# Kernel tuning notes

Measured on AMD Instinct MI355X. Metric: run time of the kernel, lower is better.

Reference implementation:

```python
import jax, jax.numpy as jnp
import numpy as np
import math

M = 0.2
S = 30.0
COS_M = math.cos(M)
SIN_M = math.sin(M)
TH = math.cos(math.pi - M)
MM = math.sin(math.pi - M) * M


def setup_inputs() -> dict:
    key = jax.random.key(0)
    k1, k2, k3 = jax.random.split(key, 3)
    B, D, C = 1024, 192, 100000
    x = jax.random.normal(k1, (B, D), dtype=jnp.float32)
    weight = jax.random.normal(k2, (C, D), dtype=jnp.float32)
    label = jax.random.randint(k3, (B,), 0, C, dtype=jnp.int64)
    return {"x": x, "weight": weight, "label": label}


def _l2norm(v, axis=-1, eps=1e-12):
    # matches F.normalize(p=2): v / max(||v||, eps)
    n = jnp.sqrt(jnp.sum(v * v, axis=axis, keepdims=True))
    return v / jnp.maximum(n, eps)


def reference(x, weight, label):
    B = x.shape[0]
    cosine = _l2norm(x) @ _l2norm(weight).T            # [B, C]
    sine = jnp.sqrt(jnp.clip(1.0 - cosine * cosine, 0.0, 1.0))
    phi = cosine * COS_M - sine * SIN_M
    phi = jnp.where(cosine - TH > 0, phi, cosine - MM)
    one_hot = jax.nn.one_hot(label, cosine.shape[1], dtype=cosine.dtype)
    output = (one_hot * phi + (1.0 - one_hot) * cosine) * S
    # cross entropy (mean reduction)
    logp = jax.nn.log_softmax(output, axis=-1)
    loss = -jnp.mean(jnp.take_along_axis(logp, label[:, None], axis=1)[:, 0])
    # top-1 accuracy (percent), detached metric
    pred = jnp.argmax(output, axis=-1)
    prec1 = jnp.mean((pred == label).astype(jnp.float32)) * 100.0
    return loss, prec1
```

## Files before the change

### kernel.cpp

```cpp
#include <hip/hip_runtime.h>
#include <math.h>

#define B_ROWS   1024
#define DIM      192
#define NCLS     100000
#define S_SCALE  30.0f
#define COS_M    0.98006657784124163f
#define SIN_M    0.19866933079506122f
#define TH_C     (-0.98006657784124163f)
#define MM_C     0.039733866159012243f
#define L2E30    43.2808512266689f
#define EXPM30   9.357622968840175e-14f
#define LN2_C    0.69314718055994531f

#define NTILE_B  784
#define NCHUNKR  16
#define ASEG_CH  1536
#define NSLOT    1568

#define NCHUNKC  1568
#define CSPLIT   128
#define NSLOT2   128
#define PACK_WGRID 3136
#define PACK_GRID  3168

typedef float floatx4 __attribute__((ext_vector_type(4)));
typedef __bf16 bf16x8 __attribute__((ext_vector_type(8)));

#define AS1 __attribute__((address_space(1)))
#define AS3 __attribute__((address_space(3)))

__device__ __forceinline__ unsigned int f2bf(float x) {
    unsigned int u = __float_as_uint(x);
    u = (u + 0x7fffu + ((u >> 16) & 1u)) >> 16;
    return u;
}
__device__ __forceinline__ unsigned int pack2(float lo, float hi) {
    return f2bf(lo) | (f2bf(hi) << 16);
}
__device__ __forceinline__ float fexp2(float x) {
#if __has_builtin(__builtin_amdgcn_exp2f)
    return __builtin_amdgcn_exp2f(x);
#else
    float r; __asm__("v_exp_f32 %0, %1" : "=v"(r) : "v"(x)); return r;
#endif
}
template <int N>
__device__ __forceinline__ float ror16(float x) {
    return __int_as_float(__builtin_amdgcn_mov_dpp(
        __float_as_int(x), 0x120 | N, 0xF, 0xF, false));
}
__device__ __forceinline__ void gload_lds16(const void* g, void* l) {
    __builtin_amdgcn_global_load_lds(
        (const AS1 unsigned int*)g, (AS3 unsigned int*)l, 16, 0, 0);
}


__global__ __launch_bounds__(256)
void pack2_kernel(const float* __restrict__ x, const float* __restrict__ w,
                  unsigned short* __restrict__ asw, unsigned short* __restrict__ wsw,
                  float* __restrict__ accum)
{
    __shared__ uint4 lds_pk[32][25];
    const int bid = blockIdx.x;
    const int t = threadIdx.x;
    const int r = t >> 3, oct = t & 7;

    const float* src;
    unsigned short* dstc;
    int rowbase, half;
    bool wside;
    if (bid < PACK_WGRID) {
        const int k = bid & 7, j = bid >> 3;
        int cs, cc, h;
        if (j < 104) {
            const int i = j / 26; h = j % 26;
            cs = k + 8 * i;  cc = cs * 13 + (h >> 1);
        } else {
            const int j2 = j - 104;
            const int i = 4 + j2 / 24; h = j2 % 24;
            cs = k + 8 * i;  cc = 416 + (cs - 32) * 12 + (h >> 1);
        }
        half = h & 1;
        rowbase = cc * 64 + half * 32;
        src = w;  dstc = wsw + (size_t)cc * 12288;  wside = true;
    } else {
        const int xb = bid - PACK_WGRID;
        half = xb & 1;
        rowbase = xb * 32;
        src = x;  dstc = asw + (size_t)(xb >> 1) * 12288;  wside = false;
        if (bid == PACK_WGRID && t < 4) accum[t] = 0.0f;
    }

    const int row = rowbase + r;
    const bool live = !wside || (row < NCLS);
    float4 buf[6];
    float s = 0.f;
    if (live) {
        const float4* sp = (const float4*)(src + (size_t)row * DIM) + oct * 6;
        #pragma unroll
        for (int q = 0; q < 6; ++q) {
            float4 v = sp[q];
            buf[q] = v;
            s += v.x * v.x + v.y * v.y + v.z * v.z + v.w * v.w;
        }
    } else {
        #pragma unroll
        for (int q = 0; q < 6; ++q) buf[q] = make_float4(0.f, 0.f, 0.f, 0.f);
    }
    s += __shfl_xor(s, 1);
    s += __shfl_xor(s, 2);
    s += __shfl_xor(s, 4);
    float inv = live ? (1.0f / fmaxf(sqrtf(s), 1e-12f)) : 0.0f;
    if (!wside) inv *= L2E30;

    #pragma unroll
    for (int j = 0; j < 3; ++j) {
        const int k8 = oct * 3 + j;
        uint4 o;
        float4 a0 = buf[2 * j], a1 = buf[2 * j + 1];
        o.x = pack2(a0.x * inv, a0.y * inv);
        o.y = pack2(a0.z * inv, a0.w * inv);
        o.z = pack2(a1.x * inv, a1.y * inv);
        o.w = pack2(a1.z * inv, a1.w * inv);
        lds_pk[r][k8] = o;
    }
    __syncthreads();
    #pragma unroll
    for (int j = 0; j < 3; ++j) {
        const int flat = j * 256 + t;
        const int sseg = flat >> 5, rr = flat & 31;
        *(uint4*)(dstc + ((size_t)(sseg * 64) + half * 32 + rr) * 8)
            = lds_pk[rr][sseg];
    }
}

__global__ __launch_bounds__(256, 2)
void gemm_stats8_kernel(const unsigned short* __restrict__ asw,
                        const unsigned short* __restrict__ wsw,
                        float2* __restrict__ pslot)
{
    __shared__ __align__(16) char lds[49152];
    const int bid  = blockIdx.x;
    const int cs   = bid & 127;
    const int rb   = bid >> 7;
    const int tid  = threadIdx.x;
    const int wv   = tid >> 6;
    const int lane = tid & 63;
    const int quad = lane >> 4, mrow = lane & 15;

    bf16x8 xfr[4][6];
    {
        const unsigned short* ab = asw + (size_t)(rb * 4 + wv) * 12288;
        #pragma unroll
        for (int a = 0; a < 4; ++a)
            #pragma unroll
            for (int ks = 0; ks < 6; ++ks)
                xfr[a][ks] = *(const bf16x8*)(ab +
                    (size_t)((ks * 4 + quad) * 64 + a * 16 + mrow) * 8);
    }

    const int nch = 12 + (cs < 32 ? 1 : 0);
    const char* wp0 = (const char*)(wsw
                    + (size_t)(cs * 12 + (cs < 32 ? cs : 32)) * 12288);

    float s_acc[4][4];
    float m_acc[4][4];
    #pragma unroll
    for (int a = 0; a < 4; ++a)
        #pragma unroll
        for (int r = 0; r < 4; ++r) { s_acc[a][r] = 0.f; m_acc[a][r] = -1e30f; }

    {
        const char* g = wp0 + wv * 6144 + lane * 16;
        char* l = lds + wv * 6144;
        #pragma unroll
        for (int i = 0; i < 6; ++i)
            gload_lds16(g + i * 1024, l + i * 1024);
    }
    __syncthreads();

    #pragma unroll 1
    for (int c = 0; c < nch; ++c) {
        if (c + 1 < nch) {
            const char* g = wp0 + (size_t)(c + 1) * 24576 + wv * 6144 + lane * 16;
            char* l = lds + ((c + 1) & 1) * 24576 + wv * 6144;
            #pragma unroll
            for (int i = 0; i < 6; ++i)
                gload_lds16(g + i * 1024, l + i * 1024);
        }

        const char* bb = lds + (c & 1) * 24576;
        floatx4 acc[4][4];
        #pragma unroll
        for (int a = 0; a < 4; ++a)
            #pragma unroll
            for (int ni = 0; ni < 4; ++ni) {
                floatx4 z = {0.f, 0.f, 0.f, 0.f};
                acc[a][ni] = z;
            }
        #pragma unroll
        for (int ks = 0; ks < 6; ++ks) {
            const char* sb = bb + (size_t)((ks * 4 + quad) * 64 + mrow) * 16;
            bf16x8 b0 = *(const bf16x8*)(sb);
            bf16x8 b1 = *(const bf16x8*)(sb + 256);
            bf16x8 b2 = *(const bf16x8*)(sb + 512);
            bf16x8 b3 = *(const bf16x8*)(sb + 768);
            #pragma unroll
            for (int a = 0; a < 4; ++a) {
                acc[a][0] = __builtin_amdgcn_mfma_f32_16x16x32_bf16(
                    xfr[a][ks], b0, acc[a][0], 0, 0, 0);
                acc[a][1] = __builtin_amdgcn_mfma_f32_16x16x32_bf16(
                    xfr[a][ks], b1, acc[a][1], 0, 0, 0);
                acc[a][2] = __builtin_amdgcn_mfma_f32_16x16x32_bf16(
                    xfr[a][ks], b2, acc[a][2], 0, 0, 0);
                acc[a][3] = __builtin_amdgcn_mfma_f32_16x16x32_bf16(
                    xfr[a][ks], b3, acc[a][3], 0, 0, 0);
            }
        }
        #pragma unroll
        for (int a = 0; a < 4; ++a)
            #pragma unroll
            for (int r = 0; r < 4; ++r) {
                float v0 = acc[a][0][r], v1 = acc[a][1][r];
                float v2 = acc[a][2][r], v3 = acc[a][3][r];
                m_acc[a][r] = fmaxf(fmaxf(fmaxf(fmaxf(v0, v1), v2), v3),
                                    m_acc[a][r]);
                s_acc[a][r] += (fexp2(v0) + fexp2(v1))
                             + (fexp2(v2) + fexp2(v3));
            }
        __syncthreads();
    }

    const int rowb = rb * 256 + wv * 64;
    #pragma unroll
    for (int a = 0; a < 4; ++a)
        #pragma unroll
        for (int r = 0; r < 4; ++r) {
            float s = s_acc[a][r], m = m_acc[a][r];
            s += ror16<1>(s); s += ror16<2>(s); s += ror16<4>(s); s += ror16<8>(s);
            m = fmaxf(m, ror16<1>(m)); m = fmaxf(m, ror16<2>(m));
            m = fmaxf(m, ror16<4>(m)); m = fmaxf(m, ror16<8>(m));
            if (mrow == 0)
                pslot[(size_t)cs * B_ROWS + rowb + a * 16 + quad * 4 + r] =
                    make_float2(m, s);
        }
}

__global__ __launch_bounds__(256)
void finalize2_kernel(const float2* __restrict__ pslot,
                      const float* __restrict__ x, const float* __restrict__ w,
                      const int* __restrict__ label,
                      float* __restrict__ accum, float* __restrict__ out)
{
    __shared__ float2 red[8][32];
    const int t = threadIdx.x, rr = t & 31, g = t >> 5;
    {
        const int row = blockIdx.x * 32 + rr;
        float M = -1e30f, L = 0.f;
        #pragma unroll
        for (int s = 0; s < NSLOT2 / 8; ++s) {
            float2 p = pslot[(size_t)(s * 8 + g) * B_ROWS + row];
            M = fmaxf(M, p.x);
            L += p.y;
        }
        red[g][rr] = make_float2(M, L);
    }
    __syncthreads();
    if (t < 32) {
        const int row = blockIdx.x * 32 + t;
        float Mc = -1e30f, L = 0.f;
        #pragma unroll
        for (int g2 = 0; g2 < 8; ++g2) {
            float2 p = red[g2][t];
            Mc = fmaxf(Mc, p.x);
            L += p.y;
        }

        const int lab = label[row];
        const float4* xr = (const float4*)(x + (size_t)row * DIM);
        const float4* wr = (const float4*)(w + (size_t)lab * DIM);
        float dot = 0.f, nx = 0.f, nw = 0.f;
        #pragma unroll
        for (int q = 0; q < 48; ++q) {
            float4 a = xr[q], b = wr[q];
            dot += a.x * b.x + a.y * b.y + a.z * b.z + a.w * b.w;
            nx  += a.x * a.x + a.y * a.y + a.z * a.z + a.w * a.w;
            nw  += b.x * b.x + b.y * b.y + b.z * b.z + b.w * b.w;
        }
        float cosl    = dot / fmaxf(sqrtf(nx) * sqrtf(nw), 1e-12f);
        float t_plain = S_SCALE * cosl;
        float sine    = sqrtf(fmaxf(0.f, fminf(1.f, 1.f - cosl * cosl)));
        float phi     = cosl * COS_M - sine * SIN_M;
        float modv    = ((cosl - TH_C) > 0.f) ? phi : (cosl - MM_C);
        float t_mod   = S_SCALE * modv;

        float Ladj = L * EXPM30 - __expf(t_plain - 30.0f) + __expf(t_mod - 30.0f);
        Ladj = fmaxf(Ladj, 1e-37f);
        float loss = (30.0f + logf(Ladj)) - t_mod;
        float corr = (t_mod > Mc * LN2_C) ? 1.f : 0.f;

        #pragma unroll
        for (int off = 16; off > 0; off >>= 1) {
            loss += __shfl_xor(loss, off);
            corr += __shfl_xor(corr, off);
        }
        if (t == 0) {
            atomicAdd(&accum[0], loss);
            atomicAdd(&accum[1], corr);
            __threadfence();
            int old = atomicAdd((int*)accum + 2, 1);
            if (old == (int)gridDim.x - 1) {
                float a0 = atomicAdd(&accum[0], 0.0f);
                float a1 = atomicAdd(&accum[1], 0.0f);
                out[0] = a0 * (1.0f / (float)B_ROWS);
                out[1] = a1 * (100.0f / (float)B_ROWS);
            }
        }
    }
}


__global__ __launch_bounds__(256)
void prep_kernel(const float* __restrict__ x, unsigned short* __restrict__ asw,
                 float* __restrict__ accum)
{
    const int ab = blockIdx.x;
    const int t = threadIdx.x;
    if (ab == 0 && t < 4) accum[t] = 0.0f;
    const int r = t >> 1, half = t & 1;
    const int row = ab * 128 + r;
    const int c = ab * 2 + (r >> 6);
    const int r64 = r & 63;

    float4 buf[24];
    float s = 0.f;
    const float4* sp = (const float4*)(x + (size_t)row * DIM) + half * 24;
    #pragma unroll
    for (int q = 0; q < 24; ++q) {
        float4 v = sp[q];
        buf[q] = v;
        s += v.x * v.x + v.y * v.y + v.z * v.z + v.w * v.w;
    }
    s += __shfl_xor(s, 1);
    const float inv = 1.0f / fmaxf(sqrtf(s), 1e-12f);
    #pragma unroll
    for (int j = 0; j < 12; ++j) {
        const int k8 = half * 12 + j;
        uint4 o;
        float4 a0 = buf[2 * j], a1 = buf[2 * j + 1];
        o.x = pack2(a0.x * inv, a0.y * inv);
        o.y = pack2(a0.z * inv, a0.w * inv);
        o.z = pack2(a1.x * inv, a1.y * inv);
        o.w = pack2(a1.z * inv, a1.w * inv);
        *(uint4*)(asw + ((size_t)c * ASEG_CH + k8 * 64 + r64) * 8) = o;
    }
}

__global__ __launch_bounds__(256, 3)
void gemm_stats_kernel(const float* __restrict__ w,
                       const unsigned short* __restrict__ asw,
                       unsigned int* __restrict__ pslot)
{
    __shared__ __align__(16) char lds[49152];
    const int tid  = threadIdx.x;
    const int wave = tid >> 6;
    const int lane = tid & 63;
    const int quad = lane >> 4;
    const int mrow = lane & 15;
    const int rg   = wave >> 1;
    const int cgr  = wave & 1;

    {
        const int r = tid >> 1, half = tid & 1;
        const int col = blockIdx.x * 128 + r;
        const bool live = (col < NCLS);
        float4 buf[24];
        float s = 0.f;
        if (live) {
            const float4* sp = (const float4*)(w + (size_t)col * DIM) + half * 24;
            #pragma unroll
            for (int q = 0; q < 24; ++q) {
                float4 v = sp[q];
                buf[q] = v;
                s += v.x * v.x + v.y * v.y + v.z * v.z + v.w * v.w;
            }
        }
        s += __shfl_xor(s, 1);
        const float inv = live ? (1.0f / fmaxf(sqrtf(s), 1e-12f)) : 0.0f;
        #pragma unroll
        for (int j = 0; j < 12; ++j) {
            const int k8 = half * 12 + j;
            uint4 o = make_uint4(0u, 0u, 0u, 0u);
            if (live) {
                float4 a0 = buf[2 * j], a1 = buf[2 * j + 1];
                o.x = pack2(a0.x * inv, a0.y * inv);
                o.y = pack2(a0.z * inv, a0.w * inv);
                o.z = pack2(a1.x * inv, a1.y * inv);
                o.w = pack2(a1.z * inv, a1.w * inv);
            }
            *(uint4*)(lds + (size_t)(k8 * 128 + r) * 16) = o;
        }
    }
    __syncthreads();

    bf16x8 bfr[6][4];
    #pragma unroll
    for (int ks = 0; ks < 6; ++ks)
        #pragma unroll
        for (int ni = 0; ni < 4; ++ni)
            bfr[ks][ni] = *(const bf16x8*)(lds +
                (((ks * 4 + quad) * 128) + cgr * 64 + ni * 16 + mrow) * 16);

    const int slot = blockIdx.x * 2 + cgr;
    #pragma unroll 2
    for (int c = 0; c < NCHUNKR; ++c) {
        const unsigned short* ab = asw + (size_t)c * ASEG_CH * 8;
        floatx4 acc[2][4];
        #pragma unroll
        for (int mi = 0; mi < 2; ++mi)
            #pragma unroll
            for (int ni = 0; ni < 4; ++ni) {
                floatx4 z = {0.f, 0.f, 0.f, 0.f};
                acc[mi][ni] = z;
            }
        #pragma unroll
        for (int ks = 0; ks < 6; ++ks) {
            bf16x8 a0 = *(const bf16x8*)(ab +
                (size_t)(((ks * 4 + quad) * 64) + rg * 32 + mrow) * 8);
            bf16x8 a1 = *(const bf16x8*)(ab +
                (size_t)(((ks * 4 + quad) * 64) + rg * 32 + 16 + mrow) * 8);
            #pragma unroll
            for (int ni = 0; ni < 4; ++ni)
                acc[0][ni] = __builtin_amdgcn_mfma_f32_16x16x32_bf16(
                    a0, bfr[ks][ni], acc[0][ni], 0, 0, 0);
            #pragma unroll
            for (int ni = 0; ni < 4; ++ni)
                acc[1][ni] = __builtin_amdgcn_mfma_f32_16x16x32_bf16(
                    a1, bfr[ks][ni], acc[1][ni], 0, 0, 0);
        }

        #pragma unroll
        for (int mi = 0; mi < 2; ++mi)
            #pragma unroll
            for (int r = 0; r < 4; ++r) {
                float v0 = acc[mi][0][r], v1 = acc[mi][1][r];
                float v2 = acc[mi][2][r], v3 = acc[mi][3][r];
                float m = fmaxf(fmaxf(v0, v1), fmaxf(v2, v3));
                float s = fexp2(fmaf(v0, L2E30, -L2E30))
                        + fexp2(fmaf(v1, L2E30, -L2E30))
                        + fexp2(fmaf(v2, L2E30, -L2E30))
                        + fexp2(fmaf(v3, L2E30, -L2E30));
                s += ror16<1>(s); s += ror16<2>(s);
                s += ror16<4>(s); s += ror16<8>(s);
                m = fmaxf(m, ror16<1>(m)); m = fmaxf(m, ror16<2>(m));
                m = fmaxf(m, ror16<4>(m)); m = fmaxf(m, ror16<8>(m));
                if (mrow == mi * 4 + r)
                    pslot[(size_t)slot * B_ROWS +
                          c * 64 + rg * 32 + mi * 16 + quad * 4 + r] = pack2(m, s);
            }
    }
}

__global__ __launch_bounds__(256)
void finalize_kernel(const unsigned int* __restrict__ pslot,
                     const float* __restrict__ x, const float* __restrict__ w,
                     const int* __restrict__ label,
                     float* __restrict__ accum, float* __restrict__ out)
{
    __shared__ float2 red[8][32];
    const int t = threadIdx.x, rr = t & 31, g = t >> 5;
    {
        const int row = blockIdx.x * 32 + rr;
        float M = -1e30f, L = 0.f;
        for (int s = g; s < NSLOT; s += 8) {
            unsigned int u = pslot[(size_t)s * B_ROWS + row];
            M = fmaxf(M, __uint_as_float(u << 16));
            L += __uint_as_float(u & 0xFFFF0000u);
        }
        red[g][rr] = make_float2(M, L);
    }
    __syncthreads();
    if (t < 32) {
        const int row = blockIdx.x * 32 + t;
        float Mc = -1e30f, L = 0.f;
        #pragma unroll
        for (int g2 = 0; g2 < 8; ++g2) {
            float2 p = red[g2][t];
            Mc = fmaxf(Mc, p.x);
            L += p.y;
        }

        const int lab = label[row];
        const float4* xr = (const float4*)(x + (size_t)row * DIM);
        const float4* wr = (const float4*)(w + (size_t)lab * DIM);
        float dot = 0.f, nx = 0.f, nw = 0.f;
        #pragma unroll
        for (int q = 0; q < 48; ++q) {
            float4 a = xr[q], b = wr[q];
            dot += a.x * b.x + a.y * b.y + a.z * b.z + a.w * b.w;
            nx  += a.x * a.x + a.y * a.y + a.z * a.z + a.w * a.w;
            nw  += b.x * b.x + b.y * b.y + b.z * b.z + b.w * b.w;
        }
        float cosl    = dot / fmaxf(sqrtf(nx) * sqrtf(nw), 1e-12f);
        float t_plain = S_SCALE * cosl;
        float sine    = sqrtf(fmaxf(0.f, fminf(1.f, 1.f - cosl * cosl)));
        float phi     = cosl * COS_M - sine * SIN_M;
        float modv    = ((cosl - TH_C) > 0.f) ? phi : (cosl - MM_C);
        float t_mod   = S_SCALE * modv;

        float Ladj = L - __expf(t_plain - 30.0f) + __expf(t_mod - 30.0f);
        Ladj = fmaxf(Ladj, 1e-37f);
        float loss = (30.0f + logf(Ladj)) - t_mod;
        float corr = (t_mod > S_SCALE * Mc) ? 1.f : 0.f;

        #pragma unroll
        for (int off = 16; off > 0; off >>= 1) {
            loss += __shfl_xor(loss, off);
            corr += __shfl_xor(corr, off);
        }
        if (t == 0) {
            atomicAdd(&accum[0], loss);
            atomicAdd(&accum[1], corr);
            __threadfence();
            int old = atomicAdd((int*)accum + 2, 1);
            if (old == (int)gridDim.x - 1) {
                float a0 = atomicAdd(&accum[0], 0.0f);
                float a1 = atomicAdd(&accum[1], 0.0f);
                out[0] = a0 * (1.0f / (float)B_ROWS);
                out[1] = a1 * (100.0f / (float)B_ROWS);
            }
        }
    }
}

extern "C" void kernel_launch(void* const* d_in, const int* in_sizes, int n_in,
                              void* d_out, int out_size, void* d_ws, size_t ws_size,
                              hipStream_t stream)
{
    const float* x     = (const float*)d_in[0];
    const float* w     = (const float*)d_in[1];
    const int*   label = (const int*)d_in[2];
    float* out = (float*)d_out;

    char* ws = (char*)d_ws;
    float* accum = (float*)ws;
    unsigned short* asw = (unsigned short*)(ws + 256);
    const size_t asw_bytes = (size_t)NCHUNKR * ASEG_CH * 16;

    const size_t wsw_bytes    = (size_t)NCHUNKC * 24 * 64 * 16;
    const size_t pslot2_bytes = (size_t)NSLOT2 * B_ROWS * 8;
    const size_t need_new = 256 + asw_bytes + wsw_bytes + pslot2_bytes;

    if (ws_size >= need_new) {
        unsigned short* wsw = (unsigned short*)(ws + 256 + asw_bytes);
        float2* pslot2 = (float2*)(ws + 256 + asw_bytes + wsw_bytes);
        pack2_kernel<<<dim3(PACK_GRID), dim3(256), 0, stream>>>(x, w, asw, wsw, accum);
        gemm_stats8_kernel<<<dim3(4 * CSPLIT), dim3(256), 0, stream>>>(asw, wsw, pslot2);
        finalize2_kernel<<<dim3(B_ROWS / 32), dim3(256), 0, stream>>>(
            pslot2, x, w, label, accum, out);
    } else {
        unsigned int* pslot = (unsigned int*)(ws + 256 + asw_bytes);
        prep_kernel<<<dim3(8), dim3(256), 0, stream>>>(x, asw, accum);
        gemm_stats_kernel<<<dim3(NTILE_B), dim3(256), 0, stream>>>(w, asw, pslot);
        finalize_kernel<<<dim3(B_ROWS / 32), dim3(256), 0, stream>>>(
            pslot, x, w, label, accum, out);
    }
}
```

Measured before the change: 162.3 us.

## Shrink GEMM block tile to 64 rows with 2x2 wave grid for more occupancy

The stats GEMM kernel now processes 64 batch rows per block instead of 256. Its four waves are arranged as a 2x2 grid over row halves and column halves, and the launch is four times larger. Per-wave register use shrinks, so the launch bound rises to four blocks per CU, and s_setprio is placed around the MFMA bursts. The cost is that each weight chunk is streamed from L2 four times as often, and the finalize pass must reduce twice as many partial (max, sum) slots.

```diff
diff --git a/kernel.cpp b/kernel.cpp
--- a/kernel.cpp
+++ b/kernel.cpp
@@ -20,7 +20,7 @@
 
 #define NCHUNKC  1568
 #define CSPLIT   128
-#define NSLOT2   128
+#define NSLOT2   256
 #define PACK_WGRID 3136
 #define PACK_GRID  3168
 
@@ -135,8 +135,8 @@
     }
 }
 
-__global__ __launch_bounds__(256, 2)
-void gemm_stats8_kernel(const unsigned short* __restrict__ asw,
+__global__ __launch_bounds__(256, 4)
+void gemm_stats9_kernel(const unsigned short* __restrict__ asw,
                         const unsigned short* __restrict__ wsw,
                         float2* __restrict__ pslot)
 {
@@ -146,28 +146,30 @@
     const int rb   = bid >> 7;
     const int tid  = threadIdx.x;
     const int wv   = tid >> 6;
+    const int rg   = wv >> 1;
+    const int cg   = wv & 1;
     const int lane = tid & 63;
     const int quad = lane >> 4, mrow = lane & 15;
 
-    bf16x8 xfr[4][6];
+    bf16x8 xfr[2][6];
     {
-        const unsigned short* ab = asw + (size_t)(rb * 4 + wv) * 12288;
-        #pragma unroll
-        for (int a = 0; a < 4; ++a)
+        const unsigned short* ab = asw + (size_t)rb * 12288;
+        #pragma unroll
+        for (int a = 0; a < 2; ++a)
             #pragma unroll
             for (int ks = 0; ks < 6; ++ks)
                 xfr[a][ks] = *(const bf16x8*)(ab +
-                    (size_t)((ks * 4 + quad) * 64 + a * 16 + mrow) * 8);
+                    (size_t)((ks * 4 + quad) * 64 + rg * 32 + a * 16 + mrow) * 8);
     }
 
     const int nch = 12 + (cs < 32 ? 1 : 0);
     const char* wp0 = (const char*)(wsw
                     + (size_t)(cs * 12 + (cs < 32 ? cs : 32)) * 12288);
 
-    float s_acc[4][4];
-    float m_acc[4][4];
-    #pragma unroll
-    for (int a = 0; a < 4; ++a)
+    float s_acc[2][4];
+    float m_acc[2][4];
+    #pragma unroll
+    for (int a = 0; a < 2; ++a)
         #pragma unroll
         for (int r = 0; r < 4; ++r) { s_acc[a][r] = 0.f; m_acc[a][r] = -1e30f; }
 
@@ -191,50 +193,46 @@
         }
 
         const char* bb = lds + (c & 1) * 24576;
-        floatx4 acc[4][4];
-        #pragma unroll
-        for (int a = 0; a < 4; ++a)
-            #pragma unroll
-            for (int ni = 0; ni < 4; ++ni) {
+        floatx4 acc[2][2];
+        #pragma unroll
+        for (int a = 0; a < 2; ++a)
+            #pragma unroll
+            for (int ni = 0; ni < 2; ++ni) {
                 floatx4 z = {0.f, 0.f, 0.f, 0.f};
                 acc[a][ni] = z;
             }
         #pragma unroll
         for (int ks = 0; ks < 6; ++ks) {
-            const char* sb = bb + (size_t)((ks * 4 + quad) * 64 + mrow) * 16;
+            const char* sb = bb
+                + (size_t)((ks * 4 + quad) * 64 + cg * 32 + mrow) * 16;
             bf16x8 b0 = *(const bf16x8*)(sb);
             bf16x8 b1 = *(const bf16x8*)(sb + 256);
-            bf16x8 b2 = *(const bf16x8*)(sb + 512);
-            bf16x8 b3 = *(const bf16x8*)(sb + 768);
-            #pragma unroll
-            for (int a = 0; a < 4; ++a) {
-                acc[a][0] = __builtin_amdgcn_mfma_f32_16x16x32_bf16(
-                    xfr[a][ks], b0, acc[a][0], 0, 0, 0);
-                acc[a][1] = __builtin_amdgcn_mfma_f32_16x16x32_bf16(
-                    xfr[a][ks], b1, acc[a][1], 0, 0, 0);
-                acc[a][2] = __builtin_amdgcn_mfma_f32_16x16x32_bf16(
-                    xfr[a][ks], b2, acc[a][2], 0, 0, 0);
-                acc[a][3] = __builtin_amdgcn_mfma_f32_16x16x32_bf16(
-                    xfr[a][ks], b3, acc[a][3], 0, 0, 0);
-            }
-        }
-        #pragma unroll
-        for (int a = 0; a < 4; ++a)
+            __builtin_amdgcn_s_setprio(1);
+            acc[0][0] = __builtin_amdgcn_mfma_f32_16x16x32_bf16(
+                xfr[0][ks], b0, acc[0][0], 0, 0, 0);
+            acc[0][1] = __builtin_amdgcn_mfma_f32_16x16x32_bf16(
+                xfr[0][ks], b1, acc[0][1], 0, 0, 0);
+            acc[1][0] = __builtin_amdgcn_mfma_f32_16x16x32_bf16(
+                xfr[1][ks], b0, acc[1][0], 0, 0, 0);
+            acc[1][1] = __builtin_amdgcn_mfma_f32_16x16x32_bf16(
+                xfr[1][ks], b1, acc[1][1], 0, 0, 0);
+            __builtin_amdgcn_s_setprio(0);
+        }
+        #pragma unroll
+        for (int a = 0; a < 2; ++a)
             #pragma unroll
             for (int r = 0; r < 4; ++r) {
                 float v0 = acc[a][0][r], v1 = acc[a][1][r];
-                float v2 = acc[a][2][r], v3 = acc[a][3][r];
-                m_acc[a][r] = fmaxf(fmaxf(fmaxf(fmaxf(v0, v1), v2), v3),
-                                    m_acc[a][r]);
-                s_acc[a][r] += (fexp2(v0) + fexp2(v1))
-                             + (fexp2(v2) + fexp2(v3));
+                m_acc[a][r] = fmaxf(fmaxf(v0, v1), m_acc[a][r]);
+                s_acc[a][r] += fexp2(v0) + fexp2(v1);
             }
         __syncthreads();
     }
 
-    const int rowb = rb * 256 + wv * 64;
-    #pragma unroll
-    for (int a = 0; a < 4; ++a)
+    const int rowb = rb * 64 + rg * 32;
+    const int sidx = cs * 2 + cg;
+    #pragma unroll
+    for (int a = 0; a < 2; ++a)
         #pragma unroll
         for (int r = 0; r < 4; ++r) {
             float s = s_acc[a][r], m = m_acc[a][r];
@@ -242,7 +240,7 @@
             m = fmaxf(m, ror16<1>(m)); m = fmaxf(m, ror16<2>(m));
             m = fmaxf(m, ror16<4>(m)); m = fmaxf(m, ror16<8>(m));
             if (mrow == 0)
-                pslot[(size_t)cs * B_ROWS + rowb + a * 16 + quad * 4 + r] =
+                pslot[(size_t)sidx * B_ROWS + rowb + a * 16 + quad * 4 + r] =
                     make_float2(m, s);
         }
 }
@@ -556,7 +554,7 @@
         unsigned short* wsw = (unsigned short*)(ws + 256 + asw_bytes);
         float2* pslot2 = (float2*)(ws + 256 + asw_bytes + wsw_bytes);
         pack2_kernel<<<dim3(PACK_GRID), dim3(256), 0, stream>>>(x, w, asw, wsw, accum);
-        gemm_stats8_kernel<<<dim3(4 * CSPLIT), dim3(256), 0, stream>>>(asw, wsw, pslot2);
+        gemm_stats9_kernel<<<dim3(16 * CSPLIT), dim3(256), 0, stream>>>(asw, wsw, pslot2);
         finalize2_kernel<<<dim3(B_ROWS / 32), dim3(256), 0, stream>>>(
             pslot2, x, w, label, accum, out);
     } else {
```

Result: slower. 169.2 us (+4.3%).

## Triple-buffer weight tiles in LDS with explicit vmcnt waits and MFMA priority

Applied to the files above, without the earlier changes.

Moves the GEMM+softmax-stats kernel's weight staging from a double buffer to a three-stage LDS ring, prefetching two chunks ahead. The full __syncthreads is replaced by counted s_waitcnt vmcnt plus raw s_barrier, so only the current chunk's loads must land. s_setprio is raised around the MFMA bursts. The aim is to hide global-to-LDS latency. LDS per block grows from 48KB to 72KB, which may limit the two-blocks-per-CU occupancy requested in launch bounds.

```diff
diff --git a/kernel.cpp b/kernel.cpp
--- a/kernel.cpp
+++ b/kernel.cpp
@@ -53,6 +53,12 @@
 __device__ __forceinline__ void gload_lds16(const void* g, void* l) {
     __builtin_amdgcn_global_load_lds(
         (const AS1 unsigned int*)g, (AS3 unsigned int*)l, 16, 0, 0);
+}
+__device__ __forceinline__ void waitcnt_vm(int pend) {
+    if (pend >= 2)      asm volatile("s_waitcnt vmcnt(12)" ::: "memory");
+    else if (pend == 1) asm volatile("s_waitcnt vmcnt(6)"  ::: "memory");
+    else                asm volatile("s_waitcnt vmcnt(0)"  ::: "memory");
+    __builtin_amdgcn_sched_barrier(0);
 }
 
 
@@ -136,11 +142,11 @@
 }
 
 __global__ __launch_bounds__(256, 2)
-void gemm_stats8_kernel(const unsigned short* __restrict__ asw,
-                        const unsigned short* __restrict__ wsw,
-                        float2* __restrict__ pslot)
-{
-    __shared__ __align__(16) char lds[49152];
+void gemm_stats10_kernel(const unsigned short* __restrict__ asw,
+                         const unsigned short* __restrict__ wsw,
+                         float2* __restrict__ pslot)
+{
+    __shared__ __align__(16) char lds[73728];
     const int bid  = blockIdx.x;
     const int cs   = bid & 127;
     const int rb   = bid >> 7;
@@ -163,6 +169,8 @@
     const int nch = 12 + (cs < 32 ? 1 : 0);
     const char* wp0 = (const char*)(wsw
                     + (size_t)(cs * 12 + (cs < 32 ? cs : 32)) * 12288);
+    const int soff = wv * 6144 + lane * 16;
+    const int loff = wv * 6144;
 
     float s_acc[4][4];
     float m_acc[4][4];
@@ -172,25 +180,30 @@
         for (int r = 0; r < 4; ++r) { s_acc[a][r] = 0.f; m_acc[a][r] = -1e30f; }
 
     {
-        const char* g = wp0 + wv * 6144 + lane * 16;
-        char* l = lds + wv * 6144;
+        const char* g0 = wp0 + soff;
         #pragma unroll
         for (int i = 0; i < 6; ++i)
-            gload_lds16(g + i * 1024, l + i * 1024);
-    }
-    __syncthreads();
+            gload_lds16(g0 + i * 1024, lds + loff + i * 1024);
+        const char* g1 = wp0 + 24576 + soff;
+        #pragma unroll
+        for (int i = 0; i < 6; ++i)
+            gload_lds16(g1 + i * 1024, lds + 24576 + loff + i * 1024);
+    }
 
     #pragma unroll 1
     for (int c = 0; c < nch; ++c) {
-        if (c + 1 < nch) {
-            const char* g = wp0 + (size_t)(c + 1) * 24576 + wv * 6144 + lane * 16;
-            char* l = lds + ((c + 1) & 1) * 24576 + wv * 6144;
+        if (c + 2 < nch) {
+            const char* g = wp0 + (size_t)(c + 2) * 24576 + soff;
+            char* l = lds + ((c + 2) % 3) * 24576 + loff;
             #pragma unroll
             for (int i = 0; i < 6; ++i)
                 gload_lds16(g + i * 1024, l + i * 1024);
         }
-
-        const char* bb = lds + (c & 1) * 24576;
+        int pend = nch - 1 - c; if (pend > 2) pend = 2;
+        waitcnt_vm(pend);
+        __builtin_amdgcn_s_barrier();
+
+        const char* bb = lds + (c % 3) * 24576;
         floatx4 acc[4][4];
         #pragma unroll
         for (int a = 0; a < 4; ++a)
@@ -206,6 +219,7 @@
             bf16x8 b1 = *(const bf16x8*)(sb + 256);
             bf16x8 b2 = *(const bf16x8*)(sb + 512);
             bf16x8 b3 = *(const bf16x8*)(sb + 768);
+            __builtin_amdgcn_s_setprio(1);
             #pragma unroll
             for (int a = 0; a < 4; ++a) {
                 acc[a][0] = __builtin_amdgcn_mfma_f32_16x16x32_bf16(
@@ -217,6 +231,7 @@
                 acc[a][3] = __builtin_amdgcn_mfma_f32_16x16x32_bf16(
                     xfr[a][ks], b3, acc[a][3], 0, 0, 0);
             }
+            __builtin_amdgcn_s_setprio(0);
         }
         #pragma unroll
         for (int a = 0; a < 4; ++a)
@@ -229,7 +244,7 @@
                 s_acc[a][r] += (fexp2(v0) + fexp2(v1))
                              + (fexp2(v2) + fexp2(v3));
             }
-        __syncthreads();
+        __builtin_amdgcn_s_barrier();
     }
 
     const int rowb = rb * 256 + wv * 64;
@@ -556,7 +571,7 @@
         unsigned short* wsw = (unsigned short*)(ws + 256 + asw_bytes);
         float2* pslot2 = (float2*)(ws + 256 + asw_bytes + wsw_bytes);
         pack2_kernel<<<dim3(PACK_GRID), dim3(256), 0, stream>>>(x, w, asw, wsw, accum);
-        gemm_stats8_kernel<<<dim3(4 * CSPLIT), dim3(256), 0, stream>>>(asw, wsw, pslot2);
+        gemm_stats10_kernel<<<dim3(4 * CSPLIT), dim3(256), 0, stream>>>(asw, wsw, pslot2);
         finalize2_kernel<<<dim3(B_ROWS / 32), dim3(256), 0, stream>>>(
             pslot2, x, w, label, accum, out);
     } else {
```

Result: no change. 159.3 us, median of 2 (-1.8%).
